# Optimization experiments

Measured on AMD Instinct MI355X. Metric: run time of the kernel, lower is better.

The kernel has to match this reference:

```python
import jax, jax.numpy as jnp
import numpy as np

NUM_CAPSULE = 16
DIM_CAPSULE = 64
ROUTINGS = 4
SEQ_LEN, BATCH, HIDDEN = 512, 64, 1024  # hidden = 2*num_hiddens (bidirectional)


def squash(x, axis=-1):
    s = jnp.sum(x * x, axis=axis, keepdims=True)
    return x / jnp.sqrt(s + 1e-7)


def setup_inputs() -> dict:
    key = jax.random.key(0)
    k1, k2 = jax.random.split(key)
    inputs = jax.random.normal(k1, (SEQ_LEN, BATCH, HIDDEN), dtype=jnp.float32)
    # xavier-normal std = sqrt(2/(fan_in+fan_out)) = sqrt(2/(1024+1024))
    std = float(np.sqrt(2.0 / (HIDDEN + NUM_CAPSULE * DIM_CAPSULE)))
    W = jax.random.normal(k2, (1, HIDDEN, NUM_CAPSULE * DIM_CAPSULE), dtype=jnp.float32) * std
    return {"inputs": inputs, "W": W}


def reference(inputs, W):
    # inputs: (S, B, H) -> (B, S, H)
    x = jnp.transpose(inputs, (1, 0, 2))
    B, S, H = x.shape
    # projection: (B,S,H) @ (H, nc*dc) -> (B,S,nc*dc)
    u = jnp.einsum('bsh,ho->bso', x, W[0])
    u = u.reshape(B, S, NUM_CAPSULE, DIM_CAPSULE)
    u = jnp.transpose(u, (0, 2, 1, 3))  # (B, nc, S, dc)
    b = jnp.zeros((B, NUM_CAPSULE, S, 1), dtype=x.dtype)
    outputs = None
    for i in range(ROUTINGS):
        c = jax.nn.softmax(b, axis=1)  # softmax over capsules
        outputs = squash(jnp.sum(c * u, axis=2))  # (B, nc, dc)
        if i < ROUTINGS - 1:
            update = jnp.sum(outputs[:, :, None, :] * u, axis=-1, keepdims=True)
            b = b + update
    return outputs
```

## Files before the change

kernel.cpp:

```cpp
#include <hip/hip_runtime.h>

typedef unsigned short u16;
typedef __attribute__((ext_vector_type(4))) float f32x4;
typedef __attribute__((ext_vector_type(8))) unsigned short u16x8;
typedef __attribute__((ext_vector_type(8))) short s16x8;

__device__ __forceinline__ u16 f2bf(float f) {
    unsigned u = __float_as_uint(f);
    u += 0x7FFFu + ((u >> 16) & 1u);
    return (u16)(u >> 16);
}
__device__ __forceinline__ float bf2f(u16 h) {
    return __uint_as_float(((unsigned)h) << 16);
}
__device__ __forceinline__ void gload_lds16(const void* g, void* l) {
    __builtin_amdgcn_global_load_lds(
        (const __attribute__((address_space(1))) unsigned int*)g,
        (__attribute__((address_space(3))) unsigned int*)l, 16, 0, 0);
}

__global__ void wtrans_k(const float* __restrict__ W, u16* __restrict__ Wt) {
    __shared__ float tile[32][33];
    const int k0 = blockIdx.x << 5, n0 = blockIdx.y << 5;
    const int tx = threadIdx.x & 31, ty = threadIdx.x >> 5;
#pragma unroll
    for (int r = 0; r < 32; r += 8)
        tile[ty + r][tx] = W[(size_t)(k0 + ty + r) * 1024 + n0 + tx];
    __syncthreads();
#pragma unroll
    for (int r = 0; r < 32; r += 8)
        Wt[(size_t)(n0 + ty + r) * 1024 + k0 + tx] = f2bf(tile[tx][ty + r]);
}

__global__ void gemm_k(const float* __restrict__ X, const u16* __restrict__ Wt,
                       u16* __restrict__ U, float* __restrict__ W0) {
    __shared__ u16 lds[16384];
    const int tid = threadIdx.x;
    const int lane = tid & 63, wave = tid >> 6;
    const int swz = (int)blockIdx.x;
    const int orig = ((swz & 7) << 8) + (swz >> 3);
    const int tm = orig >> 3, tn = orig & 7;
    const int r0 = tm << 7, c0 = tn << 7;
    const int wm = wave >> 1, wn = wave & 1;

    const int arow = tid >> 1, ahalf = tid & 1;
    const int s_ = (r0 + arow) & 511, b_ = (r0 + arow) >> 9;
    const float* asrc = X + ((size_t)s_ * 64 + b_) * 1024 + (ahalf << 4);
    const int sOff = (arow << 5) + (ahalf << 4);

    const u16* bg0 = Wt + ((size_t)(c0 + (tid >> 2)) << 10) + ((tid & 3) << 3);
    const u16* bg1 = bg0 + (size_t)(64 << 10);
    const int bOff = (wave << 9);

    const int lrow = lane & 15, lk = (lane >> 4) << 3;
    f32x4 acc[4][4] = {};

    {
        const f32x4* ap = (const f32x4*)asrc;
        f32x4 A0 = ap[0], A1 = ap[1], A2 = ap[2], A3 = ap[3];
        gload_lds16(bg0, &lds[8192 + bOff]);
        gload_lds16(bg1, &lds[8192 + bOff + 2048]);
        u16x8 pa0, pa1;
#pragma unroll
        for (int j = 0; j < 4; ++j) {
            pa0[j] = f2bf(A0[j]); pa0[4 + j] = f2bf(A1[j]);
            pa1[j] = f2bf(A2[j]); pa1[4 + j] = f2bf(A3[j]);
        }
        *(u16x8*)&lds[sOff] = pa0; *(u16x8*)&lds[sOff + 8] = pa1;
    }
    __syncthreads();

#pragma unroll 2
    for (int kt = 0; kt < 32; ++kt) {
        const int cur = kt & 1, nxt = cur ^ 1;
        f32x4 A0, A1, A2, A3;
        const bool has_next = (kt < 31);
        if (has_next) {
            const int k0e = (kt + 1) << 5;
            const f32x4* ap = (const f32x4*)(asrc + k0e);
            A0 = ap[0]; A1 = ap[1]; A2 = ap[2]; A3 = ap[3];
            gload_lds16(bg0 + k0e, &lds[8192 + nxt * 4096 + bOff]);
            gload_lds16(bg1 + k0e, &lds[8192 + nxt * 4096 + bOff + 2048]);
        }
        const u16* sA = lds + cur * 4096;
        const u16* sB = lds + 8192 + cur * 4096;
        s16x8 af[4], bfr[4];
#pragma unroll
        for (int m = 0; m < 4; ++m)
            af[m] = *(const s16x8*)&sA[((wm << 6) + (m << 4) + lrow) * 32 + lk];
#pragma unroll
        for (int n = 0; n < 4; ++n)
            bfr[n] = *(const s16x8*)&sB[((wn << 6) + (n << 4) + lrow) * 32 + lk];
#pragma unroll
        for (int m = 0; m < 4; ++m)
#pragma unroll
            for (int n = 0; n < 4; ++n)
                acc[m][n] = __builtin_amdgcn_mfma_f32_16x16x32_bf16(af[m], bfr[n], acc[m][n], 0, 0, 0);
        if (has_next) {
            u16x8 pa0, pa1;
#pragma unroll
            for (int j = 0; j < 4; ++j) {
                pa0[j] = f2bf(A0[j]); pa0[4 + j] = f2bf(A1[j]);
                pa1[j] = f2bf(A2[j]); pa1[4 + j] = f2bf(A3[j]);
            }
            u16* dA = lds + nxt * 4096;
            *(u16x8*)&dA[sOff] = pa0; *(u16x8*)&dA[sOff + 8] = pa1;
        }
        __syncthreads();
    }

    u16* sC = lds;
#pragma unroll
    for (int m = 0; m < 4; ++m)
#pragma unroll
        for (int n = 0; n < 4; ++n)
#pragma unroll
            for (int j = 0; j < 4; ++j) {
                const int row = (wm << 6) + (m << 4) + ((lane >> 4) << 2) + j;
                const int col = (wn << 6) + (n << 4) + (lane & 15);
                sC[(row << 7) + col] = f2bf(acc[m][n][j]);
            }
    {
        const int bb = tm >> 2;
#pragma unroll
        for (int n = 0; n < 4; ++n) {
            float p = 0.f;
#pragma unroll
            for (int m = 0; m < 4; ++m)
#pragma unroll
                for (int j = 0; j < 4; ++j) p += acc[m][n][j];
            p += __shfl_xor(p, 16);
            p += __shfl_xor(p, 32);
            if (lane < 16)
                atomicAdd(&W0[(bb << 10) + c0 + (wn << 6) + (n << 4) + lane], p);
        }
    }
    __syncthreads();
    const int orow = tid >> 1, ocol = (tid & 1) << 6;
    u16* gdst = U + ((size_t)(r0 + orow) << 10) + c0 + ocol;
    const u16* sp = sC + (orow << 7) + ocol;
#pragma unroll
    for (int q = 0; q < 8; ++q)
        *(u16x8*)(gdst + (q << 3)) = *(const u16x8*)(sp + (q << 3));
}

__global__ void squash_k(const float* __restrict__ Win, float* __restrict__ Vout) {
    const int g = (blockIdx.x << 2) + (threadIdx.x >> 6);
    const int lane = threadIdx.x & 63;
    float x = Win[((size_t)g << 6) + lane];
    float s = x * x;
#pragma unroll
    for (int d = 1; d < 64; d <<= 1) s += __shfl_xor(s, d);
    Vout[((size_t)g << 6) + lane] = x / sqrtf(s + 1e-7f);
}

__global__ void route_pass(const u16* __restrict__ U, const float* __restrict__ V,
                           float* __restrict__ Bbuf, float* __restrict__ Wout,
                           const int hasB, const int writeB) {
    const int tid = threadIdx.x;
    const int wave = tid >> 6, lane = tid & 63;
    const int b = blockIdx.y, bx = blockIdx.x;
    const int grp = lane >> 2, sub = lane & 3;
    __shared__ float wlds[4 * 64 * 20];
    float v[16];
    const float* vp = V + (size_t)((b << 4) + grp) * 64 + (sub << 4);
#pragma unroll
    for (int j = 0; j < 16; ++j) v[j] = vp[j];
    float wacc[16] = {};
    const int s0 = (bx << 5) + (wave << 3);
    const size_t rbase0 = (size_t)(b << 9) + s0;
    const u16* ubase = U + (rbase0 << 10) + (lane << 4);

    u16x8 cv0[4], cv1[4], nv0[4], nv1[4];
#pragma unroll
    for (int r = 0; r < 4; ++r) {
        const u16x8* up = (const u16x8*)(ubase + ((size_t)r << 10));
        cv0[r] = up[0]; cv1[r] = up[1];
    }
#pragma unroll
    for (int half = 0; half < 2; ++half) {
        if (half == 0) {
#pragma unroll
            for (int r = 0; r < 4; ++r) {
                const u16x8* up = (const u16x8*)(ubase + ((size_t)(r + 4) << 10));
                nv0[r] = up[0]; nv1[r] = up[1];
            }
        }
#pragma unroll
        for (int r = 0; r < 4; ++r) {
            const int s = s0 + (half << 2) + r;
            const size_t rb = (size_t)(b << 9) + s;
            float uf[16];
#pragma unroll
            for (int j = 0; j < 8; ++j) { uf[j] = bf2f(cv0[r][j]); uf[8 + j] = bf2f(cv1[r][j]); }
            float p = 0.f;
#pragma unroll
            for (int j = 0; j < 16; ++j) p = fmaf(uf[j], v[j], p);
            p += __shfl_xor(p, 1);
            p += __shfl_xor(p, 2);
            float bn = p;
            if (hasB) bn += Bbuf[(rb << 4) + grp];
            float mx = bn;
#pragma unroll
            for (int d = 4; d < 64; d <<= 1) mx = fmaxf(mx, __shfl_xor(mx, d));
            float e = __expf(bn - mx);
            float sm = e;
#pragma unroll
            for (int d = 4; d < 64; d <<= 1) sm += __shfl_xor(sm, d);
            const float c = e / sm;
            if (writeB && sub == 0) Bbuf[(rb << 4) + grp] = bn;
#pragma unroll
            for (int j = 0; j < 16; ++j) wacc[j] = fmaf(c, uf[j], wacc[j]);
        }
        if (half == 0) {
#pragma unroll
            for (int r = 0; r < 4; ++r) { cv0[r] = nv0[r]; cv1[r] = nv1[r]; }
        }
    }
    const int rowb = ((wave << 6) + lane) * 20;
#pragma unroll
    for (int j = 0; j < 16; ++j) wlds[rowb + j] = wacc[j];
    __syncthreads();
#pragma unroll
    for (int c = 0; c < 4; ++c) {
        const int q = tid + (c << 8);
        const int l = q >> 4, j = q & 15;
        float s = 0.f;
#pragma unroll
        for (int w = 0; w < 4; ++w) s += wlds[((w << 6) + l) * 20 + j];
        atomicAdd(&Wout[((size_t)b << 10) + q], s);
    }
}

#define WS_U   ((size_t)0)
#define WS_WT  ((size_t)67108864)
#define WS_W   ((size_t)69206016)
#define WS_V   ((size_t)70254592)
#define WS_B   ((size_t)71041024)

extern "C" void kernel_launch(void* const* d_in, const int* in_sizes, int n_in,
                              void* d_out, int out_size, void* d_ws, size_t ws_size,
                              hipStream_t stream) {
    (void)in_sizes; (void)n_in; (void)out_size; (void)ws_size;
    const float* x = (const float*)d_in[0];
    const float* W = (const float*)d_in[1];
    float* out = (float*)d_out;
    char* ws = (char*)d_ws;
    u16* U = (u16*)(ws + WS_U);
    u16* Wt = (u16*)(ws + WS_WT);
    float* wbuf = (float*)(ws + WS_W);
    float* vbuf = (float*)(ws + WS_V);
    float* bbuf = (float*)(ws + WS_B);

    hipMemsetAsync(wbuf, 0, 4 * 65536 * sizeof(float), stream);
    wtrans_k<<<dim3(32, 32), 256, 0, stream>>>(W, Wt);
    gemm_k<<<2048, 256, 0, stream>>>(x, Wt, U, wbuf);
    squash_k<<<256, 256, 0, stream>>>(wbuf, vbuf);
    route_pass<<<dim3(16, 64), 256, 0, stream>>>(U, vbuf, bbuf, wbuf + 65536, 0, 1);
    squash_k<<<256, 256, 0, stream>>>(wbuf + 65536, vbuf + 65536);
    route_pass<<<dim3(16, 64), 256, 0, stream>>>(U, vbuf + 65536, bbuf, wbuf + 2 * 65536, 1, 1);
    squash_k<<<256, 256, 0, stream>>>(wbuf + 2 * 65536, vbuf + 2 * 65536);
    route_pass<<<dim3(16, 64), 256, 0, stream>>>(U, vbuf + 2 * 65536, bbuf, wbuf + 3 * 65536, 1, 0);
    squash_k<<<256, 256, 0, stream>>>(wbuf + 3 * 65536, out);
}
```

Before: 407.0 us.

## Pre-convert X to bf16, load both GEMM operands via LDS DMA, drop routing atomics

A new kernel converts and transposes the fp32 activations to a bf16 row-major buffer before the GEMM, so the GEMM streams both operands straight into LDS with global_load_lds instead of converting A in registers. The routing pass now writes per-block partial sums to a buffer that a new squash kernel reduces, replacing global atomics and most of the memset. It also removes the softmax max-subtraction and uses a fast reciprocal. The cost is an extra full pass over X (read fp32, write bf16) and a larger workspace, and the softmax without max subtraction relies on logits staying small.

New measurement: 394.1 us. 3.2% less time.

```diff
diff --git a/kernel.cpp b/kernel.cpp
--- a/kernel.cpp
+++ b/kernel.cpp
@@ -19,6 +19,20 @@
         (__attribute__((address_space(3))) unsigned int*)l, 16, 0, 0);
 }
 
+__global__ void xcvt_k(const float* __restrict__ X, u16* __restrict__ Xb) {
+    const int t = (int)(blockIdx.x * 256 + threadIdx.x);
+    const int orow = t >> 7;
+    const int col = (t & 127) << 3;
+    const int b = orow >> 9, s = orow & 511;
+    const float* src = X + (((size_t)s << 6) + b) * 1024 + col;
+    f32x4 x0 = *(const f32x4*)src;
+    f32x4 x1 = *(const f32x4*)(src + 4);
+    u16x8 o;
+#pragma unroll
+    for (int j = 0; j < 4; ++j) { o[j] = f2bf(x0[j]); o[4 + j] = f2bf(x1[j]); }
+    *(u16x8*)(Xb + ((size_t)orow << 10) + col) = o;
+}
+
 __global__ void wtrans_k(const float* __restrict__ W, u16* __restrict__ Wt) {
     __shared__ float tile[32][33];
     const int k0 = blockIdx.x << 5, n0 = blockIdx.y << 5;
@@ -32,7 +46,7 @@
         Wt[(size_t)(n0 + ty + r) * 1024 + k0 + tx] = f2bf(tile[tx][ty + r]);
 }
 
-__global__ void gemm_k(const float* __restrict__ X, const u16* __restrict__ Wt,
+__global__ void gemm_k(const u16* __restrict__ Xb, const u16* __restrict__ Wt,
                        u16* __restrict__ U, float* __restrict__ W0) {
     __shared__ u16 lds[16384];
     const int tid = threadIdx.x;
@@ -43,44 +57,30 @@
     const int r0 = tm << 7, c0 = tn << 7;
     const int wm = wave >> 1, wn = wave & 1;
 
-    const int arow = tid >> 1, ahalf = tid & 1;
-    const int s_ = (r0 + arow) & 511, b_ = (r0 + arow) >> 9;
-    const float* asrc = X + ((size_t)s_ * 64 + b_) * 1024 + (ahalf << 4);
-    const int sOff = (arow << 5) + (ahalf << 4);
-
+    const u16* ag0 = Xb + ((size_t)(r0 + (tid >> 2)) << 10) + ((tid & 3) << 3);
+    const u16* ag1 = ag0 + ((size_t)64 << 10);
     const u16* bg0 = Wt + ((size_t)(c0 + (tid >> 2)) << 10) + ((tid & 3) << 3);
-    const u16* bg1 = bg0 + (size_t)(64 << 10);
-    const int bOff = (wave << 9);
+    const u16* bg1 = bg0 + ((size_t)64 << 10);
+    const int sOff = wave << 9;
 
     const int lrow = lane & 15, lk = (lane >> 4) << 3;
     f32x4 acc[4][4] = {};
 
-    {
-        const f32x4* ap = (const f32x4*)asrc;
-        f32x4 A0 = ap[0], A1 = ap[1], A2 = ap[2], A3 = ap[3];
-        gload_lds16(bg0, &lds[8192 + bOff]);
-        gload_lds16(bg1, &lds[8192 + bOff + 2048]);
-        u16x8 pa0, pa1;
-#pragma unroll
-        for (int j = 0; j < 4; ++j) {
-            pa0[j] = f2bf(A0[j]); pa0[4 + j] = f2bf(A1[j]);
-            pa1[j] = f2bf(A2[j]); pa1[4 + j] = f2bf(A3[j]);
-        }
-        *(u16x8*)&lds[sOff] = pa0; *(u16x8*)&lds[sOff + 8] = pa1;
-    }
+    gload_lds16(ag0, &lds[sOff]);
+    gload_lds16(ag1, &lds[sOff + 2048]);
+    gload_lds16(bg0, &lds[8192 + sOff]);
+    gload_lds16(bg1, &lds[8192 + sOff + 2048]);
     __syncthreads();
 
 #pragma unroll 2
     for (int kt = 0; kt < 32; ++kt) {
         const int cur = kt & 1, nxt = cur ^ 1;
-        f32x4 A0, A1, A2, A3;
-        const bool has_next = (kt < 31);
-        if (has_next) {
-            const int k0e = (kt + 1) << 5;
-            const f32x4* ap = (const f32x4*)(asrc + k0e);
-            A0 = ap[0]; A1 = ap[1]; A2 = ap[2]; A3 = ap[3];
-            gload_lds16(bg0 + k0e, &lds[8192 + nxt * 4096 + bOff]);
-            gload_lds16(bg1 + k0e, &lds[8192 + nxt * 4096 + bOff + 2048]);
+        if (kt < 31) {
+            const int ke = (kt + 1) << 5;
+            gload_lds16(ag0 + ke, &lds[nxt * 4096 + sOff]);
+            gload_lds16(ag1 + ke, &lds[nxt * 4096 + sOff + 2048]);
+            gload_lds16(bg0 + ke, &lds[8192 + nxt * 4096 + sOff]);
+            gload_lds16(bg1 + ke, &lds[8192 + nxt * 4096 + sOff + 2048]);
         }
         const u16* sA = lds + cur * 4096;
         const u16* sB = lds + 8192 + cur * 4096;
@@ -96,16 +96,6 @@
 #pragma unroll
             for (int n = 0; n < 4; ++n)
                 acc[m][n] = __builtin_amdgcn_mfma_f32_16x16x32_bf16(af[m], bfr[n], acc[m][n], 0, 0, 0);
-        if (has_next) {
-            u16x8 pa0, pa1;
-#pragma unroll
-            for (int j = 0; j < 4; ++j) {
-                pa0[j] = f2bf(A0[j]); pa0[4 + j] = f2bf(A1[j]);
-                pa1[j] = f2bf(A2[j]); pa1[4 + j] = f2bf(A3[j]);
-            }
-            u16* dA = lds + nxt * 4096;
-            *(u16x8*)&dA[sOff] = pa0; *(u16x8*)&dA[sOff + 8] = pa1;
-        }
         __syncthreads();
     }
 
@@ -154,8 +144,22 @@
     Vout[((size_t)g << 6) + lane] = x / sqrtf(s + 1e-7f);
 }
 
+__global__ void squash16_k(const float* __restrict__ WP, float* __restrict__ Vout) {
+    const int g = (blockIdx.x << 2) + (threadIdx.x >> 6);
+    const int lane = threadIdx.x & 63;
+    const int b = g >> 4, i = g & 15;
+    const float* p = WP + (((size_t)b) << 10) + (i << 6) + lane;
+    float x = 0.f;
+#pragma unroll
+    for (int c = 0; c < 16; ++c) x += p[((size_t)c) << 16];
+    float s = x * x;
+#pragma unroll
+    for (int d = 1; d < 64; d <<= 1) s += __shfl_xor(s, d);
+    Vout[((size_t)g << 6) + lane] = x / sqrtf(s + 1e-7f);
+}
+
 __global__ void route_pass(const u16* __restrict__ U, const float* __restrict__ V,
-                           float* __restrict__ Bbuf, float* __restrict__ Wout,
+                           float* __restrict__ Bbuf, float* __restrict__ WP,
                            const int hasB, const int writeB) {
     const int tid = threadIdx.x;
     const int wave = tid >> 6, lane = tid & 63;
@@ -171,56 +175,43 @@
     const size_t rbase0 = (size_t)(b << 9) + s0;
     const u16* ubase = U + (rbase0 << 10) + (lane << 4);
 
-    u16x8 cv0[4], cv1[4], nv0[4], nv1[4];
-#pragma unroll
-    for (int r = 0; r < 4; ++r) {
+    u16x8 rv[16];
+#pragma unroll
+    for (int r = 0; r < 8; ++r) {
         const u16x8* up = (const u16x8*)(ubase + ((size_t)r << 10));
-        cv0[r] = up[0]; cv1[r] = up[1];
-    }
-#pragma unroll
-    for (int half = 0; half < 2; ++half) {
-        if (half == 0) {
-#pragma unroll
-            for (int r = 0; r < 4; ++r) {
-                const u16x8* up = (const u16x8*)(ubase + ((size_t)(r + 4) << 10));
-                nv0[r] = up[0]; nv1[r] = up[1];
-            }
+        rv[2 * r] = up[0];
+        rv[2 * r + 1] = up[1];
+    }
+#pragma unroll
+    for (int r = 0; r < 8; ++r) {
+        const size_t rb = rbase0 + r;
+        float uf[16];
+#pragma unroll
+        for (int j = 0; j < 8; ++j) {
+            uf[j] = bf2f(rv[2 * r][j]);
+            uf[8 + j] = bf2f(rv[2 * r + 1][j]);
         }
-#pragma unroll
-        for (int r = 0; r < 4; ++r) {
-            const int s = s0 + (half << 2) + r;
-            const size_t rb = (size_t)(b << 9) + s;
-            float uf[16];
-#pragma unroll
-            for (int j = 0; j < 8; ++j) { uf[j] = bf2f(cv0[r][j]); uf[8 + j] = bf2f(cv1[r][j]); }
-            float p = 0.f;
-#pragma unroll
-            for (int j = 0; j < 16; ++j) p = fmaf(uf[j], v[j], p);
-            p += __shfl_xor(p, 1);
-            p += __shfl_xor(p, 2);
-            float bn = p;
-            if (hasB) bn += Bbuf[(rb << 4) + grp];
-            float mx = bn;
-#pragma unroll
-            for (int d = 4; d < 64; d <<= 1) mx = fmaxf(mx, __shfl_xor(mx, d));
-            float e = __expf(bn - mx);
-            float sm = e;
-#pragma unroll
-            for (int d = 4; d < 64; d <<= 1) sm += __shfl_xor(sm, d);
-            const float c = e / sm;
-            if (writeB && sub == 0) Bbuf[(rb << 4) + grp] = bn;
-#pragma unroll
-            for (int j = 0; j < 16; ++j) wacc[j] = fmaf(c, uf[j], wacc[j]);
-        }
-        if (half == 0) {
-#pragma unroll
-            for (int r = 0; r < 4; ++r) { cv0[r] = nv0[r]; cv1[r] = nv1[r]; }
-        }
+        float p = 0.f;
+#pragma unroll
+        for (int j = 0; j < 16; ++j) p = fmaf(uf[j], v[j], p);
+        p += __shfl_xor(p, 1);
+        p += __shfl_xor(p, 2);
+        float bn = p;
+        if (hasB) bn += Bbuf[(rb << 4) + grp];
+        float e = __expf(bn);
+        float sm = e;
+#pragma unroll
+        for (int d = 4; d < 64; d <<= 1) sm += __shfl_xor(sm, d);
+        const float c = e * __builtin_amdgcn_rcpf(sm);
+        if (writeB && sub == 0) Bbuf[(rb << 4) + grp] = bn;
+#pragma unroll
+        for (int j = 0; j < 16; ++j) wacc[j] = fmaf(c, uf[j], wacc[j]);
     }
     const int rowb = ((wave << 6) + lane) * 20;
 #pragma unroll
     for (int j = 0; j < 16; ++j) wlds[rowb + j] = wacc[j];
     __syncthreads();
+    float* wpdst = WP + (((size_t)(bx << 6) + b) << 10);
 #pragma unroll
     for (int c = 0; c < 4; ++c) {
         const int q = tid + (c << 8);
@@ -228,15 +219,17 @@
         float s = 0.f;
 #pragma unroll
         for (int w = 0; w < 4; ++w) s += wlds[((w << 6) + l) * 20 + j];
-        atomicAdd(&Wout[((size_t)b << 10) + q], s);
+        wpdst[q] = s;
     }
 }
 
 #define WS_U   ((size_t)0)
-#define WS_WT  ((size_t)67108864)
-#define WS_W   ((size_t)69206016)
-#define WS_V   ((size_t)70254592)
-#define WS_B   ((size_t)71041024)
+#define WS_XB  ((size_t)67108864)
+#define WS_WP  ((size_t)67108864)
+#define WS_BB  ((size_t)71303168)
+#define WS_WT  ((size_t)134217728)
+#define WS_W0  ((size_t)136314880)
+#define WS_V   ((size_t)136577024)
 
 extern "C" void kernel_launch(void* const* d_in, const int* in_sizes, int n_in,
                               void* d_out, int out_size, void* d_ws, size_t ws_size,
@@ -247,19 +240,24 @@
     float* out = (float*)d_out;
     char* ws = (char*)d_ws;
     u16* U = (u16*)(ws + WS_U);
+    u16* Xb = (u16*)(ws + WS_XB);
     u16* Wt = (u16*)(ws + WS_WT);
-    float* wbuf = (float*)(ws + WS_W);
-    float* vbuf = (float*)(ws + WS_V);
-    float* bbuf = (float*)(ws + WS_B);
-
-    hipMemsetAsync(wbuf, 0, 4 * 65536 * sizeof(float), stream);
+    float* w0 = (float*)(ws + WS_W0);
+    float* v0 = (float*)(ws + WS_V);
+    float* v1 = v0 + 65536;
+    float* v2 = v1 + 65536;
+    float* wp = (float*)(ws + WS_WP);
+    float* bb = (float*)(ws + WS_BB);
+
+    hipMemsetAsync(w0, 0, 65536 * sizeof(float), stream);
     wtrans_k<<<dim3(32, 32), 256, 0, stream>>>(W, Wt);
-    gemm_k<<<2048, 256, 0, stream>>>(x, Wt, U, wbuf);
-    squash_k<<<256, 256, 0, stream>>>(wbuf, vbuf);
-    route_pass<<<dim3(16, 64), 256, 0, stream>>>(U, vbuf, bbuf, wbuf + 65536, 0, 1);
-    squash_k<<<256, 256, 0, stream>>>(wbuf + 65536, vbuf + 65536);
-    route_pass<<<dim3(16, 64), 256, 0, stream>>>(U, vbuf + 65536, bbuf, wbuf + 2 * 65536, 1, 1);
-    squash_k<<<256, 256, 0, stream>>>(wbuf + 2 * 65536, vbuf + 2 * 65536);
-    route_pass<<<dim3(16, 64), 256, 0, stream>>>(U, vbuf + 2 * 65536, bbuf, wbuf + 3 * 65536, 1, 0);
-    squash_k<<<256, 256, 0, stream>>>(wbuf + 3 * 65536, out);
-}
+    xcvt_k<<<16384, 256, 0, stream>>>(x, Xb);
+    gemm_k<<<2048, 256, 0, stream>>>(Xb, Wt, U, w0);
+    squash_k<<<256, 256, 0, stream>>>(w0, v0);
+    route_pass<<<dim3(16, 64), 256, 0, stream>>>(U, v0, bb, wp, 0, 1);
+    squash16_k<<<256, 256, 0, stream>>>(wp, v1);
+    route_pass<<<dim3(16, 64), 256, 0, stream>>>(U, v1, bb, wp, 1, 1);
+    squash16_k<<<256, 256, 0, stream>>>(wp, v2);
+    route_pass<<<dim3(16, 64), 256, 0, stream>>>(U, v2, bb, wp, 1, 0);
+    squash16_k<<<256, 256, 0, stream>>>(wp, out);
+}
```
